# Kernel tuning notes

Measured on AMD Instinct MI355X. Metric: run time of the kernel, lower is better.

## Reference

```python
import jax, jax.numpy as jnp
import numpy as np

DT = 0.001          # continuous-dynamics step (dt > 0 branch)
KERNEL_SIZE = 16384 # L
P, H = 1024, 256    # d_state, d_input (= d_output)


def setup_inputs() -> dict:
    key = jax.random.key(0)
    kAr, kAi, kB, kC = jax.random.split(key, 4)
    # Continuous diagonal state matrix: real part in [strong, weak] = [-0.5, -0.01] (stable),
    # imaginary part uniform in [-pi, pi] (mimics diagonal_state_space_matrix init).
    Ar = jax.random.uniform(kAr, (P,), minval=-0.5, maxval=-0.01)
    Ai = jax.random.uniform(kAi, (P,), minval=-np.pi, maxval=np.pi)
    A = jnp.stack([Ar, Ai], axis=-1).astype(jnp.float32)            # (P, 2) view_as_real
    # B, C ~ uniform disk (radius 1): scaled complex gaussians are a fine stand-in numerically.
    B = (jax.random.normal(kB, (P, H, 2)) / np.sqrt(H)).astype(jnp.float32)   # (P, H, 2)
    C = (jax.random.normal(kC, (H, P, 2)) / np.sqrt(P)).astype(jnp.float32)   # (H, P, 2)
    return {"A": A, "B": B, "C": C}


def _as_complex(x):
    return x[..., 0] + 1j * x[..., 1]


def reference(A, B, C):
    """Vandermonde SSM kernel generation (continuous dt > 0 branch).
    Returns kernel (H, L, 2) = real view of complex kernel (H, L)."""
    Ac = _as_complex(A)   # (P,) complex
    Bc = _as_complex(B)   # (P, H)
    Cc = _as_complex(C)   # (H, P)

    # ZOH-style discretization
    A_bar = jnp.exp(Ac * DT)                               # (P,)
    B_bar = ((A_bar - 1.0) / Ac)[:, None] * Bc             # (P, H)

    # Vandermonde matrix V[p, l] = A_bar[p] ** l  (complex power == exp(l * log(a)))
    powers = jnp.arange(KERNEL_SIZE, dtype=jnp.float32)    # (L,)
    V = jnp.exp(jnp.log(A_bar)[:, None] * powers[None, :]) # (P, L)

    # W[h, p] = C[h, p] * B_bar[p, h]; kernel[h, l] = sum_p W[h, p] * V[p, l]
    W = Cc * B_bar.T                                       # (H, P)
    kernel = jnp.einsum('hp,pl->hl', W, V)                 # (H, L) complex
    return jnp.stack([kernel.real, kernel.imag], axis=-1)  # (H, L, 2) float32
```

## Files before the change

### kernel.cpp

```cpp
#include <hip/hip_runtime.h>
#include <hip/hip_fp16.h>

#define P_DIM 1024
#define H_DIM 256
#define L_DIM 16384
#define DT 0.001f
#define TWOPI 6.283185307179586f
#define INV2PI 0.15915494309189535f
#define WSCALE 4096.0f
#define INV_WSCALE (1.0f / 4096.0f)
#define BM 128
#define BN 256
#define BK 64
#define NT 512

typedef _Float16 f16x8 __attribute__((ext_vector_type(8)));
typedef float f32x4 __attribute__((ext_vector_type(4)));

#define GPTR(p) (const __attribute__((address_space(1))) unsigned*)(p)
#define LPTR(p) (__attribute__((address_space(3))) unsigned*)(p)

union H2U { __half2 h; unsigned u; };

__device__ __forceinline__ float2 cmulf(float2 a, float2 b) {
    return make_float2(a.x * b.x - a.y * b.y, a.x * b.y + a.y * b.x);
}

__global__ __launch_bounds__(256)
void prep_kernel(const float* __restrict__ Ag, const float* __restrict__ Bg,
                 const float* __restrict__ Cg, __half* __restrict__ W2) {
    __shared__ float2 Bt[64][33];
    __shared__ float2 sc[64];
    const int t  = threadIdx.x;
    const int p0 = (blockIdx.x & 15) << 6;
    const int h0 = (blockIdx.x >> 4) << 5;

    if (t < 64) {
        float2 a = ((const float2*)Ag)[p0 + t];
        float er = __expf(a.x * DT);
        float s, c; __sincosf(a.y * DT, &s, &c);
        float nr = er * c - 1.f, ni = er * s;
        float inv = 1.f / (a.x * a.x + a.y * a.y);
        sc[t] = make_float2((nr * a.x + ni * a.y) * inv, (ni * a.x - nr * a.y) * inv);
    }
    #pragma unroll
    for (int i = 0; i < 8; ++i) {
        int idx = i * 256 + t, p = idx >> 5, h = idx & 31;
        Bt[p][h] = ((const float2*)Bg)[(size_t)(p0 + p) * H_DIM + h0 + h];
    }
    __syncthreads();
    #pragma unroll
    for (int i = 0; i < 8; ++i) {
        int idx = i * 256 + t, h = idx >> 6, p = idx & 63;
        float2 cc = ((const float2*)Cg)[(size_t)(h0 + h) * P_DIM + p0 + p];
        float2 s2 = sc[p], b = Bt[p][h];
        float2 tv = cmulf(cc, s2);
        float wr = (tv.x * b.x - tv.y * b.y) * WSCALE;
        float wi = (tv.x * b.y + tv.y * b.x) * WSCALE;
        ((__half2*)W2)[(size_t)(h0 + h) * P_DIM + p0 + p] =
            __float22half2_rn(make_float2(wr, wi));
    }
}

__global__ __launch_bounds__(NT, 2)
void vand_mfma_kernel(const float* __restrict__ Ag,
                      const _Float16* __restrict__ W2,
                      float* __restrict__ out) {
    __shared__ __attribute__((aligned(16))) _Float16 As[2][BM * BK];
    __shared__ __attribute__((aligned(16))) _Float16 Bs[2][BN * BK];
    __shared__ float4 Atab[P_DIM];

    const int tid  = threadIdx.x;
    const int lane = tid & 63;
    const int w    = tid >> 6;
    const int wm   = w & 1, wn = w >> 1;
    const int m0   = blockIdx.y * BM;
    const int nb   = blockIdx.x * BN;
    const int lb   = blockIdx.x * (BN / 2);

    const float2* Ag2 = (const float2*)Ag;

    #pragma unroll
    for (int i = 0; i < 2; ++i) {
        int p = tid + i * 512;
        float2 a = Ag2[p];
        float e = __expf(a.x * DT);
        float s, c; __sincosf(a.y * DT, &s, &c);
        Atab[p] = make_float4(e * c, e * s, a.x * DT, a.y * (DT * INV2PI));
    }

    f32x4 acc[4][4];
    #pragma unroll
    for (int mt = 0; mt < 4; ++mt)
        #pragma unroll
        for (int nt = 0; nt < 4; ++nt)
            acc[mt][nt] = (f32x4){0.f, 0.f, 0.f, 0.f};

    const int pl    = tid & 31;
    const int lg    = tid >> 5;
    const float l0f = (float)(lb + lg * 8);
    const int cq3   = (pl >> 2) << 3;
    const int cs    = (2 * pl) & 7;
    const int vbase = lg * 1024 + cs;

    const int goff = (lane >> 3) * 2048 + (((lane & 7) ^ (lane >> 3)) << 3);
    const _Float16* gwbase = W2 + (size_t)(m0 + (w << 4)) * 2048;
    const int ldsoff = (w << 4) * 64;

    _Float16* Acur = &As[0][0]; _Float16* Bcur = &Bs[0][0];
    _Float16* Anxt = &As[1][0]; _Float16* Bnxt = &Bs[1][0];

    float2 vv, ab;

#define DMA_CHUNK(K0, DST)                                                        \
    {                                                                             \
        const _Float16* gw = gwbase + (K0) + goff;                                \
        _Float16* lB = (DST) + ldsoff;                                            \
        _Pragma("unroll")                                                         \
        for (int r = 0; r < 2; ++r)                                               \
            __builtin_amdgcn_global_load_lds(GPTR(gw + r * 8 * 2048),             \
                                             LPTR(lB + r * 8 * 64), 16, 0, 0);    \
    }

#define VGEN_ANCHOR(K0)                                                           \
    {                                                                             \
        const int pg = ((K0) >> 1) + pl;                                          \
        float4 t4 = Atab[pg];                                                     \
        float mg = __expf(t4.z * l0f);                                            \
        float x  = t4.w * l0f; x -= rintf(x);                                     \
        float s, c; __sincosf(x * TWOPI, &s, &c);                                 \
        vv = make_float2(mg * c, mg * s);                                         \
        ab = make_float2(t4.x, t4.y);                                             \
    }

#define VGEN_J(DST, J)                                                            \
    {                                                                             \
        H2U u0, u1;                                                               \
        u0.h = __float22half2_rn(make_float2(vv.x, -vv.y));                       \
        u1.h = __float22half2_rn(make_float2(vv.y, vv.x));                        \
        int e0 = vbase + (J) * 128 + (cq3 ^ (((2 * (J)) & 7) << 3));              \
        int e1 = vbase + (J) * 128 + 64 + (cq3 ^ (((2 * (J) + 1) & 7) << 3));     \
        *(unsigned*)((DST) + e0) = u0.u;                                          \
        *(unsigned*)((DST) + e1) = u1.u;                                          \
        vv = cmulf(vv, ab);                                                       \
    }

#define FRAG_READS(KS)                                                            \
    {                                                                             \
        const int g = (KS) * 4 + (lane >> 4);                                     \
        _Pragma("unroll")                                                         \
        for (int t = 0; t < 4; ++t) {                                             \
            int m = wm * 64 + t * 16 + (lane & 15);                               \
            af[t] = *(const f16x8*)(Acur + m * 64 + ((g ^ (m & 7)) << 3));        \
            int n = wn * 64 + t * 16 + (lane & 15);                               \
            bf[t] = *(const f16x8*)(Bcur + n * 64 + ((g ^ (n & 7)) << 3));        \
        }                                                                         \
    }

#define MFMA_CLUSTER                                                              \
    __builtin_amdgcn_s_setprio(1);                                                \
    _Pragma("unroll")                                                             \
    for (int mt = 0; mt < 4; ++mt)                                                \
        _Pragma("unroll")                                                         \
        for (int nt = 0; nt < 4; ++nt)                                            \
            acc[mt][nt] = __builtin_amdgcn_mfma_f32_16x16x32_f16(                 \
                af[mt], bf[nt], acc[mt][nt], 0, 0, 0);                            \
    __builtin_amdgcn_s_setprio(0);

    DMA_CHUNK(0, Acur)
    __syncthreads();
    VGEN_ANCHOR(0)
    VGEN_J(Bcur, 0) VGEN_J(Bcur, 1) VGEN_J(Bcur, 2) VGEN_J(Bcur, 3)
    VGEN_J(Bcur, 4) VGEN_J(Bcur, 5) VGEN_J(Bcur, 6) VGEN_J(Bcur, 7)
    asm volatile("s_waitcnt lgkmcnt(0)" ::: "memory");
    __builtin_amdgcn_sched_barrier(0);
    __builtin_amdgcn_s_barrier();
    __builtin_amdgcn_sched_barrier(0);

    for (int kk = 0; kk < 32; ++kk) {
        {
            f16x8 af[4], bf[4];
            FRAG_READS(0)
            if (kk < 31) {
                DMA_CHUNK((kk + 1) * BK, Anxt)
                VGEN_ANCHOR((kk + 1) * BK)
                VGEN_J(Bnxt, 0) VGEN_J(Bnxt, 1) VGEN_J(Bnxt, 2) VGEN_J(Bnxt, 3)
            }
            __builtin_amdgcn_sched_barrier(0);
            __builtin_amdgcn_s_barrier();
            asm volatile("s_waitcnt lgkmcnt(0)" ::: "memory");
            __builtin_amdgcn_sched_barrier(0);
            MFMA_CLUSTER
            __builtin_amdgcn_sched_barrier(0);
            __builtin_amdgcn_s_barrier();
            __builtin_amdgcn_sched_barrier(0);
        }
        {
            f16x8 af[4], bf[4];
            FRAG_READS(1)
            if (kk < 31) {
                VGEN_J(Bnxt, 4) VGEN_J(Bnxt, 5) VGEN_J(Bnxt, 6) VGEN_J(Bnxt, 7)
            }
            asm volatile("s_waitcnt vmcnt(0)" ::: "memory");
            __builtin_amdgcn_sched_barrier(0);
            __builtin_amdgcn_s_barrier();
            asm volatile("s_waitcnt lgkmcnt(0)" ::: "memory");
            __builtin_amdgcn_sched_barrier(0);
            MFMA_CLUSTER
            __builtin_amdgcn_sched_barrier(0);
            __builtin_amdgcn_s_barrier();
            __builtin_amdgcn_sched_barrier(0);
        }
        _Float16* tA = Acur; Acur = Anxt; Anxt = tA;
        _Float16* tB = Bcur; Bcur = Bnxt; Bnxt = tB;
    }

    #pragma unroll
    for (int mt = 0; mt < 4; ++mt) {
        #pragma unroll
        for (int nt = 0; nt < 4; ++nt) {
            int h = m0 + wm * 64 + mt * 16 + ((lane >> 4) << 2);
            int n = nb + wn * 64 + nt * 16 + (lane & 15);
            #pragma unroll
            for (int r = 0; r < 4; ++r)
                out[(size_t)(h + r) * 32768 + n] = acc[mt][nt][r] * INV_WSCALE;
        }
    }
#undef DMA_CHUNK
#undef VGEN_ANCHOR
#undef VGEN_J
#undef FRAG_READS
#undef MFMA_CLUSTER
}

extern "C" void kernel_launch(void* const* d_in, const int* in_sizes, int n_in,
                              void* d_out, int out_size, void* d_ws, size_t ws_size,
                              hipStream_t stream) {
    const float* A = (const float*)d_in[0];
    const float* B = (const float*)d_in[1];
    const float* C = (const float*)d_in[2];
    float* out = (float*)d_out;
    __half* W2 = (__half*)d_ws;

    prep_kernel<<<dim3(128), dim3(256), 0, stream>>>(A, B, C, W2);
    vand_mfma_kernel<<<dim3(L_DIM * 2 / BN, H_DIM / BM), dim3(NT), 0, stream>>>(
        A, (const _Float16*)W2, out);
}
```

Before: 111.2 us.

## Split k-step into four MFMA phases with interleaved V generation and deeper A prefetch

Restructures the main loop into four smaller phases of 8 MFMAs each. Each phase interleaves LDS fragment reads and one slice of on-the-fly Vandermonde tile generation, with barriers in between. The V-generation thread mapping changes so each thread produces two p columns and writes 8-byte LDS stores. The W tile DMA is issued two chunks ahead with a partial vmcnt wait instead of a full drain. The intent is finer overlap of VALU/LDS work with MFMAs and hiding of global latency, at the cost of more barriers per k-step.

```diff
diff --git a/kernel.cpp b/kernel.cpp
--- a/kernel.cpp
+++ b/kernel.cpp
@@ -96,12 +96,11 @@
         for (int nt = 0; nt < 4; ++nt)
             acc[mt][nt] = (f32x4){0.f, 0.f, 0.f, 0.f};
 
-    const int pl    = tid & 31;
-    const int lg    = tid >> 5;
-    const float l0f = (float)(lb + lg * 8);
-    const int cq3   = (pl >> 2) << 3;
-    const int cs    = (2 * pl) & 7;
-    const int vbase = lg * 1024 + cs;
+    const int q    = tid & 15;
+    const int llq  = (tid >> 4) << 2;
+    const float l0f = (float)(lb + llq);
+    const int grp  = q >> 1, sub = (q & 1) << 2;
+    float2 vv0, vv1, ab0, ab1;
 
     const int goff = (lane >> 3) * 2048 + (((lane & 7) ^ (lane >> 3)) << 3);
     const _Float16* gwbase = W2 + (size_t)(m0 + (w << 4)) * 2048;
@@ -110,7 +109,7 @@
     _Float16* Acur = &As[0][0]; _Float16* Bcur = &Bs[0][0];
     _Float16* Anxt = &As[1][0]; _Float16* Bnxt = &Bs[1][0];
 
-    float2 vv, ab;
+    f16x8 afr[2][4];
 
 #define DMA_CHUNK(K0, DST)                                                        \
     {                                                                             \
@@ -124,93 +123,118 @@
 
 #define VGEN_ANCHOR(K0)                                                           \
     {                                                                             \
-        const int pg = ((K0) >> 1) + pl;                                          \
-        float4 t4 = Atab[pg];                                                     \
-        float mg = __expf(t4.z * l0f);                                            \
-        float x  = t4.w * l0f; x -= rintf(x);                                     \
-        float s, c; __sincosf(x * TWOPI, &s, &c);                                 \
-        vv = make_float2(mg * c, mg * s);                                         \
-        ab = make_float2(t4.x, t4.y);                                             \
-    }
-
-#define VGEN_J(DST, J)                                                            \
-    {                                                                             \
-        H2U u0, u1;                                                               \
-        u0.h = __float22half2_rn(make_float2(vv.x, -vv.y));                       \
-        u1.h = __float22half2_rn(make_float2(vv.y, vv.x));                        \
-        int e0 = vbase + (J) * 128 + (cq3 ^ (((2 * (J)) & 7) << 3));              \
-        int e1 = vbase + (J) * 128 + 64 + (cq3 ^ (((2 * (J) + 1) & 7) << 3));     \
-        *(unsigned*)((DST) + e0) = u0.u;                                          \
-        *(unsigned*)((DST) + e1) = u1.u;                                          \
-        vv = cmulf(vv, ab);                                                       \
-    }
-
-#define FRAG_READS(KS)                                                            \
+        const int pg = ((K0) >> 1) + 2 * q;                                       \
+        float4 t0 = Atab[pg], t1 = Atab[pg + 1];                                  \
+        ab0 = make_float2(t0.x, t0.y); ab1 = make_float2(t1.x, t1.y);             \
+        float s, c;                                                               \
+        float mg = __expf(t0.z * l0f);                                            \
+        float x  = t0.w * l0f; x -= rintf(x); __sincosf(x * TWOPI, &s, &c);       \
+        vv0 = make_float2(mg * c, mg * s);                                        \
+        mg = __expf(t1.z * l0f);                                                  \
+        x  = t1.w * l0f; x -= rintf(x); __sincosf(x * TWOPI, &s, &c);             \
+        vv1 = make_float2(mg * c, mg * s);                                        \
+    }
+
+#define VGEN_SLICE(J, DST)                                                        \
+    {                                                                             \
+        int n0 = 2 * (llq + (J));                                                 \
+        H2U h0u, h1u, h2u, h3u;                                                   \
+        h0u.h = __float22half2_rn(make_float2(vv0.x, -vv0.y));                    \
+        h1u.h = __float22half2_rn(make_float2(vv1.x, -vv1.y));                    \
+        h2u.h = __float22half2_rn(make_float2(vv0.y, vv0.x));                     \
+        h3u.h = __float22half2_rn(make_float2(vv1.y, vv1.x));                     \
+        int e0 = n0 * 64 + ((grp ^ (n0 & 7)) << 3) + sub;                         \
+        int e1 = (n0 + 1) * 64 + ((grp ^ ((n0 + 1) & 7)) << 3) + sub;             \
+        *(uint2*)((DST) + e0) = make_uint2(h0u.u, h1u.u);                         \
+        *(uint2*)((DST) + e1) = make_uint2(h2u.u, h3u.u);                         \
+        vv0 = cmulf(vv0, ab0); vv1 = cmulf(vv1, ab1);                             \
+    }
+
+#define RD_AF(KS)                                                                 \
     {                                                                             \
         const int g = (KS) * 4 + (lane >> 4);                                     \
         _Pragma("unroll")                                                         \
-        for (int t = 0; t < 4; ++t) {                                             \
-            int m = wm * 64 + t * 16 + (lane & 15);                               \
-            af[t] = *(const f16x8*)(Acur + m * 64 + ((g ^ (m & 7)) << 3));        \
-            int n = wn * 64 + t * 16 + (lane & 15);                               \
-            bf[t] = *(const f16x8*)(Bcur + n * 64 + ((g ^ (n & 7)) << 3));        \
+        for (int mt = 0; mt < 4; ++mt) {                                          \
+            int m = wm * 64 + mt * 16 + (lane & 15);                              \
+            afr[KS][mt] = *(const f16x8*)(Acur + m * 64 + ((g ^ (m & 7)) << 3));  \
         }                                                                         \
     }
 
-#define MFMA_CLUSTER                                                              \
+#define RD_BF(KS, NH)                                                             \
+    {                                                                             \
+        const int g = (KS) * 4 + (lane >> 4);                                     \
+        _Pragma("unroll")                                                         \
+        for (int i = 0; i < 2; ++i) {                                             \
+            int n = wn * 64 + (2 * (NH) + i) * 16 + (lane & 15);                  \
+            bf[i] = *(const f16x8*)(Bcur + n * 64 + ((g ^ (n & 7)) << 3));        \
+        }                                                                         \
+    }
+
+#define MFMA8(KS, NH)                                                             \
     __builtin_amdgcn_s_setprio(1);                                                \
     _Pragma("unroll")                                                             \
     for (int mt = 0; mt < 4; ++mt)                                                \
         _Pragma("unroll")                                                         \
-        for (int nt = 0; nt < 4; ++nt)                                            \
-            acc[mt][nt] = __builtin_amdgcn_mfma_f32_16x16x32_f16(                 \
-                af[mt], bf[nt], acc[mt][nt], 0, 0, 0);                            \
+        for (int i = 0; i < 2; ++i)                                               \
+            acc[mt][2 * (NH) + i] = __builtin_amdgcn_mfma_f32_16x16x32_f16(       \
+                afr[KS][mt], bf[i], acc[mt][2 * (NH) + i], 0, 0, 0);              \
     __builtin_amdgcn_s_setprio(0);
 
-    DMA_CHUNK(0, Acur)
+#define WAIT_LGKM                                                                 \
+    asm volatile("s_waitcnt lgkmcnt(0)" ::: "memory");                            \
+    __builtin_amdgcn_sched_barrier(0);
+
+#define BAR                                                                       \
+    __builtin_amdgcn_sched_barrier(0);                                            \
+    __builtin_amdgcn_s_barrier();                                                 \
+    __builtin_amdgcn_sched_barrier(0);
+
+    DMA_CHUNK(0, &As[0][0])
     __syncthreads();
     VGEN_ANCHOR(0)
-    VGEN_J(Bcur, 0) VGEN_J(Bcur, 1) VGEN_J(Bcur, 2) VGEN_J(Bcur, 3)
-    VGEN_J(Bcur, 4) VGEN_J(Bcur, 5) VGEN_J(Bcur, 6) VGEN_J(Bcur, 7)
-    asm volatile("s_waitcnt lgkmcnt(0)" ::: "memory");
-    __builtin_amdgcn_sched_barrier(0);
-    __builtin_amdgcn_s_barrier();
-    __builtin_amdgcn_sched_barrier(0);
-
-    for (int kk = 0; kk < 32; ++kk) {
-        {
-            f16x8 af[4], bf[4];
-            FRAG_READS(0)
-            if (kk < 31) {
-                DMA_CHUNK((kk + 1) * BK, Anxt)
-                VGEN_ANCHOR((kk + 1) * BK)
-                VGEN_J(Bnxt, 0) VGEN_J(Bnxt, 1) VGEN_J(Bnxt, 2) VGEN_J(Bnxt, 3)
-            }
+    VGEN_SLICE(0, &Bs[0][0]) VGEN_SLICE(1, &Bs[0][0])
+    VGEN_SLICE(2, &Bs[0][0]) VGEN_SLICE(3, &Bs[0][0])
+    DMA_CHUNK(BK, &As[1][0])
+    WAIT_LGKM
+    BAR
+
+    for (int t = 0; t < 32; ++t) {
+        f16x8 bf[2];
+        RD_AF(0)
+        RD_BF(0, 0)
+        if (t < 31) { VGEN_ANCHOR((t + 1) * BK) VGEN_SLICE(0, Bnxt) }
+        BAR
+        WAIT_LGKM
+        MFMA8(0, 0)
+        BAR
+        RD_BF(0, 1)
+        if (t < 31) { VGEN_SLICE(1, Bnxt) }
+        BAR
+        WAIT_LGKM
+        MFMA8(0, 1)
+        BAR
+        RD_AF(1)
+        RD_BF(1, 0)
+        if (t < 31) { VGEN_SLICE(2, Bnxt) }
+        BAR
+        WAIT_LGKM
+        MFMA8(1, 0)
+        BAR
+        RD_BF(1, 1)
+        if (t < 31) { VGEN_SLICE(3, Bnxt) }
+        if (t < 30) {
+            DMA_CHUNK((t + 2) * BK, Acur)
+            asm volatile("s_waitcnt vmcnt(2)" ::: "memory");
             __builtin_amdgcn_sched_barrier(0);
-            __builtin_amdgcn_s_barrier();
-            asm volatile("s_waitcnt lgkmcnt(0)" ::: "memory");
-            __builtin_amdgcn_sched_barrier(0);
-            MFMA_CLUSTER
-            __builtin_amdgcn_sched_barrier(0);
-            __builtin_amdgcn_s_barrier();
+        } else if (t == 30) {
+            asm volatile("s_waitcnt vmcnt(0)" ::: "memory");
             __builtin_amdgcn_sched_barrier(0);
         }
-        {
-            f16x8 af[4], bf[4];
-            FRAG_READS(1)
-            if (kk < 31) {
-                VGEN_J(Bnxt, 4) VGEN_J(Bnxt, 5) VGEN_J(Bnxt, 6) VGEN_J(Bnxt, 7)
-            }
-            asm volatile("s_waitcnt vmcnt(0)" ::: "memory");
-            __builtin_amdgcn_sched_barrier(0);
-            __builtin_amdgcn_s_barrier();
-            asm volatile("s_waitcnt lgkmcnt(0)" ::: "memory");
-            __builtin_amdgcn_sched_barrier(0);
-            MFMA_CLUSTER
-            __builtin_amdgcn_sched_barrier(0);
-            __builtin_amdgcn_s_barrier();
-            __builtin_amdgcn_sched_barrier(0);
-        }
+        BAR
+        WAIT_LGKM
+        MFMA8(1, 1)
+        BAR
+
         _Float16* tA = Acur; Acur = Anxt; Anxt = tA;
         _Float16* tB = Bcur; Bcur = Bnxt; Bnxt = tB;
     }
@@ -228,9 +252,12 @@
     }
 #undef DMA_CHUNK
 #undef VGEN_ANCHOR
-#undef VGEN_J
-#undef FRAG_READS
-#undef MFMA_CLUSTER
+#undef VGEN_SLICE
+#undef RD_AF
+#undef RD_BF
+#undef MFMA8
+#undef WAIT_LGKM
+#undef BAR
 }
 
 extern "C" void kernel_launch(void* const* d_in, const int* in_sizes, int n_in,
```

New measurement: 115.0 us. 1.03x slower.
